# Optimization experiments

Hardware: AMD Instinct MI355X
Metric: run time of the kernel (lower is better)

The kernel has to match this reference:

```python
import jax, jax.numpy as jnp
import numpy as np

THRESHOLD = 0.3

def ternary_ste(w, threshold=THRESHOLD):
    # hard threshold to {-1, 0, +1}; straight-through in bwd via stop_gradient trick
    q = jnp.where(w > threshold, 1.0, jnp.where(w < -threshold, -1.0, 0.0)).astype(w.dtype)
    return w + jax.lax.stop_gradient(q - w)

def setup_inputs() -> dict:
    key = jax.random.key(0)
    k1, k2 = jax.random.split(key)
    x = jax.random.normal(k1, (16, 4096, 512), dtype=jnp.float32)
    weight = jax.random.normal(k2, (512, 512), dtype=jnp.float32) * 0.1  # nn.Parameter(randn*0.1)
    return {"x": x, "weight": weight}

def reference(x, weight):
    qw = ternary_ste(weight)  # [out_dim, in_dim]
    # F.linear(x, W) == x @ W.T
    return jnp.einsum('bsi,oi->bso', x, qw)
```

## Files before the change

kernel.cpp:

```cpp
#include <hip/hip_runtime.h>


#define TH    0.3f
#define NSLOT 16
#define ROWS  16
#define HALF  8
#define KDIM  512
#define NDIM  512

__global__ __launch_bounds__(64) void build_tbl(const float* __restrict__ w,
                                                int* __restrict__ counts,
                                                int* __restrict__ tbl) {
    const int o    = blockIdx.x;
    const int lane = threadIdx.x;
    __shared__ int c;
    __shared__ int se[KDIM];
    if (lane == 0) c = 0;
    __syncthreads();
    const float* row = w + (size_t)o * KDIM;
    for (int i = lane; i < KDIM; i += 64) {
        float v = row[i];
        if (v > TH || v < -TH) {
            int pos = atomicAdd(&c, 1);
            se[pos] = (i << 1) | (v < 0.0f ? 1 : 0);
        }
    }
    __syncthreads();
    const int cnt = c;
    if (lane == 0) counts[o] = cnt;
    for (int k = lane; k < NSLOT; k += 64)
        tbl[o * NSLOT + k] = (k < cnt) ? se[k] : 0;
}

__global__ __launch_bounds__(512) void sort_cols(const int* __restrict__ counts,
                                                 const int* __restrict__ tbl,
                                                 int* __restrict__ perm,
                                                 int* __restrict__ scnt,
                                                 int* __restrict__ stbl) {
    const int t = threadIdx.x;
    const int cnt = counts[t];
    const int key = cnt < (NSLOT + 1) ? cnt : (NSLOT + 1);
    __shared__ int base[NSLOT + 2];
    if (t < NSLOT + 2) base[t] = 0;
    __syncthreads();
    atomicAdd(&base[key], 1);
    __syncthreads();
    if (t == 0) {
        int run = 0;
        for (int c2 = NSLOT + 1; c2 >= 0; --c2) { int h = base[c2]; base[c2] = run; run += h; }
    }
    __syncthreads();
    const int pos = atomicAdd(&base[key], 1);
    perm[pos] = t;
    scnt[pos] = cnt;
#pragma unroll
    for (int k = 0; k < NSLOT; ++k) stbl[pos * NSLOT + k] = tbl[t * NSLOT + k];
}

__global__ __launch_bounds__(512, 8) void ternary_mm(
        const float* __restrict__ x, const float* __restrict__ w,
        const int* __restrict__ perm, const int* __restrict__ scnt,
        const int* __restrict__ stbl, float* __restrict__ out, int ntiles) {
    __shared__ float xs[ROWS * KDIM];

    const int t  = threadIdx.x;
    const int c  = perm[t];
    const int ct = scnt[t];
    int e[NSLOT];
#pragma unroll
    for (int k = 0; k < NSLOT; ++k) e[k] = stbl[t * NSLOT + k];

    const int fast = (ct <= NSLOT) ? ct : 0;
    int wm = fast;
#pragma unroll
    for (int off = 32; off; off >>= 1) { int o2 = __shfl_xor(wm, off); wm = wm > o2 ? wm : o2; }
    wm = __builtin_amdgcn_readfirstlane(wm);

    for (int tile = blockIdx.x; tile < ntiles; tile += gridDim.x) {
        const size_t base = (size_t)tile * (ROWS * KDIM);

        __syncthreads();
        {
            const float4* src = (const float4*)(x + base);
            float4 st0 = src[0 * 512 + t];
            float4 st1 = src[1 * 512 + t];
            float4 st2 = src[2 * 512 + t];
            float4 st3 = src[3 * 512 + t];
            float4* dst = (float4*)xs;
            dst[0 * 512 + t] = st0;
            dst[1 * 512 + t] = st1;
            dst[2 * 512 + t] = st2;
            dst[3 * 512 + t] = st3;
        }
        __syncthreads();

#pragma unroll
        for (int h = 0; h < 2; ++h) {
            float acc[HALF];
#pragma unroll
            for (int r = 0; r < HALF; ++r) acc[r] = 0.0f;

            if (ct <= NSLOT) {
#pragma unroll
                for (int k = 0; k < NSLOT; ++k) {
                    if (k >= wm) break;
                    if (k < fast) {
                        const int ent  = e[k];
                        const int idx  = ent >> 1;
                        const int smsk = (ent & 1) << 31;
#pragma unroll
                        for (int r = 0; r < HALF; ++r) {
                            float v = xs[(h * HALF + r) * KDIM + idx];
                            acc[r] += __int_as_float(__float_as_int(v) ^ smsk);
                        }
                    }
                }
            } else {
                const float* wrow = w + (size_t)c * KDIM;
                for (int i = 0; i < KDIM; ++i) {
                    float wv = wrow[i];
                    if (wv > TH || wv < -TH) {
                        const int smsk = (wv < 0.0f) ? (1 << 31) : 0;
#pragma unroll
                        for (int r = 0; r < HALF; ++r) {
                            float v = xs[(h * HALF + r) * KDIM + i];
                            acc[r] += __int_as_float(__float_as_int(v) ^ smsk);
                        }
                    }
                }
            }

            __syncthreads();
#pragma unroll
            for (int r = 0; r < HALF; ++r)
                xs[(h * HALF + r) * KDIM + c] = acc[r];
        }
        __syncthreads();

        {
            float4* dst = (float4*)(out + base);
            const float4* s4 = (const float4*)xs;
            dst[0 * 512 + t] = s4[0 * 512 + t];
            dst[1 * 512 + t] = s4[1 * 512 + t];
            dst[2 * 512 + t] = s4[2 * 512 + t];
            dst[3 * 512 + t] = s4[3 * 512 + t];
        }
    }
}

extern "C" void kernel_launch(void* const* d_in, const int* in_sizes, int n_in,
                              void* d_out, int out_size, void* d_ws, size_t ws_size,
                              hipStream_t stream) {
    const float* x = (const float*)d_in[0];
    const float* w = (const float*)d_in[1];
    float* out = (float*)d_out;

    int* counts = (int*)d_ws;
    int* tbl    = counts + NDIM;
    int* perm   = tbl + NDIM * NSLOT;
    int* scnt   = perm + NDIM;
    int* stbl   = scnt + NDIM;

    const int nrows  = in_sizes[0] / KDIM;
    const int ntiles = nrows / ROWS;

    build_tbl<<<NDIM, 64, 0, stream>>>(w, counts, tbl);
    sort_cols<<<1, 512, 0, stream>>>(counts, tbl, perm, scnt, stbl);
    ternary_mm<<<1024, 512, 0, stream>>>(x, w, perm, scnt, stbl, out, ntiles);
}
```

Baseline: 250.0 us.

## Fuse weight prep into one kernel and process full tiles per block

The two preprocessing kernels become one single-block kernel. It uses wave ballots and popcount to build the sparse ternary tables, then sorts the output columns by nonzero count. The main kernel no longer grid-strides: it launches one block per 16-row tile and accumulates all 16 rows in one pass instead of two halves, which removes extra barriers and raises per-thread ILP. Output is written with nontemporal stores. The trade-offs are higher register pressure from 16 accumulators and a serial single-block prep that could add latency.

```diff
diff --git a/kernel.cpp b/kernel.cpp
--- a/kernel.cpp
+++ b/kernel.cpp
@@ -4,63 +4,61 @@
 #define TH    0.3f
 #define NSLOT 16
 #define ROWS  16
-#define HALF  8
 #define KDIM  512
 #define NDIM  512
 
-__global__ __launch_bounds__(64) void build_tbl(const float* __restrict__ w,
-                                                int* __restrict__ counts,
-                                                int* __restrict__ tbl) {
-    const int o    = blockIdx.x;
-    const int lane = threadIdx.x;
-    __shared__ int c;
-    __shared__ int se[KDIM];
-    if (lane == 0) c = 0;
+typedef float floatx4 __attribute__((ext_vector_type(4)));
+
+__global__ __launch_bounds__(512) void prep(const float* __restrict__ w,
+                                            int* __restrict__ perm,
+                                            int* __restrict__ scnt,
+                                            int* __restrict__ stbl,
+                                            int* __restrict__ tbl) {
+    const int t    = threadIdx.x;
+    const int lane = t & 63;
+    const int wv   = t >> 6;
+    __shared__ int counts[NDIM];
+    __shared__ int hist[NSLOT + 2];
+
+    for (int r = wv * 64; r < wv * 64 + 64; ++r) {
+        const float* row = w + (size_t)r * KDIM;
+        int cnt = 0;
+        for (int it = 0; it < 8; ++it) {
+            const int i = it * 64 + lane;
+            const float v = row[i];
+            const bool m = (v > TH) || (v < -TH);
+            const unsigned long long mask = __ballot(m);
+            if (m) {
+                int pos = cnt + __popcll(mask & ((1ull << lane) - 1ull));
+                if (pos < NSLOT) tbl[r * NSLOT + pos] = (i << 1) | (v < 0.0f ? 1 : 0);
+            }
+            cnt += __popcll(mask);
+        }
+        if (lane == 0) counts[r] = cnt;
+        if (lane >= cnt && lane < NSLOT) tbl[r * NSLOT + lane] = 0;
+    }
+    if (t < NSLOT + 2) hist[t] = 0;
     __syncthreads();
-    const float* row = w + (size_t)o * KDIM;
-    for (int i = lane; i < KDIM; i += 64) {
-        float v = row[i];
-        if (v > TH || v < -TH) {
-            int pos = atomicAdd(&c, 1);
-            se[pos] = (i << 1) | (v < 0.0f ? 1 : 0);
-        }
-    }
-    __syncthreads();
-    const int cnt = c;
-    if (lane == 0) counts[o] = cnt;
-    for (int k = lane; k < NSLOT; k += 64)
-        tbl[o * NSLOT + k] = (k < cnt) ? se[k] : 0;
-}
 
-__global__ __launch_bounds__(512) void sort_cols(const int* __restrict__ counts,
-                                                 const int* __restrict__ tbl,
-                                                 int* __restrict__ perm,
-                                                 int* __restrict__ scnt,
-                                                 int* __restrict__ stbl) {
-    const int t = threadIdx.x;
     const int cnt = counts[t];
-    const int key = cnt < (NSLOT + 1) ? cnt : (NSLOT + 1);
-    __shared__ int base[NSLOT + 2];
-    if (t < NSLOT + 2) base[t] = 0;
-    __syncthreads();
-    atomicAdd(&base[key], 1);
+    const int key = cnt < NSLOT + 1 ? cnt : NSLOT + 1;
+    atomicAdd(&hist[key], 1);
     __syncthreads();
     if (t == 0) {
         int run = 0;
-        for (int c2 = NSLOT + 1; c2 >= 0; --c2) { int h = base[c2]; base[c2] = run; run += h; }
+        for (int k = NSLOT + 1; k >= 0; --k) { int h = hist[k]; hist[k] = run; run += h; }
     }
     __syncthreads();
-    const int pos = atomicAdd(&base[key], 1);
+    const int pos = atomicAdd(&hist[key], 1);
     perm[pos] = t;
     scnt[pos] = cnt;
-#pragma unroll
     for (int k = 0; k < NSLOT; ++k) stbl[pos * NSLOT + k] = tbl[t * NSLOT + k];
 }
 
 __global__ __launch_bounds__(512, 8) void ternary_mm(
         const float* __restrict__ x, const float* __restrict__ w,
         const int* __restrict__ perm, const int* __restrict__ scnt,
-        const int* __restrict__ stbl, float* __restrict__ out, int ntiles) {
+        const int* __restrict__ stbl, float* __restrict__ out) {
     __shared__ float xs[ROWS * KDIM];
 
     const int t  = threadIdx.x;
@@ -76,75 +74,64 @@
     for (int off = 32; off; off >>= 1) { int o2 = __shfl_xor(wm, off); wm = wm > o2 ? wm : o2; }
     wm = __builtin_amdgcn_readfirstlane(wm);
 
-    for (int tile = blockIdx.x; tile < ntiles; tile += gridDim.x) {
-        const size_t base = (size_t)tile * (ROWS * KDIM);
+    const size_t base = (size_t)blockIdx.x * (ROWS * KDIM);
 
-        __syncthreads();
-        {
-            const float4* src = (const float4*)(x + base);
-            float4 st0 = src[0 * 512 + t];
-            float4 st1 = src[1 * 512 + t];
-            float4 st2 = src[2 * 512 + t];
-            float4 st3 = src[3 * 512 + t];
-            float4* dst = (float4*)xs;
-            dst[0 * 512 + t] = st0;
-            dst[1 * 512 + t] = st1;
-            dst[2 * 512 + t] = st2;
-            dst[3 * 512 + t] = st3;
-        }
-        __syncthreads();
+    {
+        const floatx4* src = (const floatx4*)(x + base);
+        floatx4 a0 = src[0 * 512 + t], a1 = src[1 * 512 + t];
+        floatx4 a2 = src[2 * 512 + t], a3 = src[3 * 512 + t];
+        floatx4* dst = (floatx4*)xs;
+        dst[0 * 512 + t] = a0; dst[1 * 512 + t] = a1;
+        dst[2 * 512 + t] = a2; dst[3 * 512 + t] = a3;
+    }
+    __syncthreads();
 
+    float acc[ROWS];
 #pragma unroll
-        for (int h = 0; h < 2; ++h) {
-            float acc[HALF];
+    for (int r = 0; r < ROWS; ++r) acc[r] = 0.0f;
+
+    if (ct <= NSLOT) {
 #pragma unroll
-            for (int r = 0; r < HALF; ++r) acc[r] = 0.0f;
-
-            if (ct <= NSLOT) {
+        for (int k = 0; k < NSLOT; ++k) {
+            if (k >= wm) break;
+            if (k < fast) {
+                const int idx = e[k] >> 1;
+                const int sm  = (e[k] & 1) << 31;
 #pragma unroll
-                for (int k = 0; k < NSLOT; ++k) {
-                    if (k >= wm) break;
-                    if (k < fast) {
-                        const int ent  = e[k];
-                        const int idx  = ent >> 1;
-                        const int smsk = (ent & 1) << 31;
-#pragma unroll
-                        for (int r = 0; r < HALF; ++r) {
-                            float v = xs[(h * HALF + r) * KDIM + idx];
-                            acc[r] += __int_as_float(__float_as_int(v) ^ smsk);
-                        }
-                    }
-                }
-            } else {
-                const float* wrow = w + (size_t)c * KDIM;
-                for (int i = 0; i < KDIM; ++i) {
-                    float wv = wrow[i];
-                    if (wv > TH || wv < -TH) {
-                        const int smsk = (wv < 0.0f) ? (1 << 31) : 0;
-#pragma unroll
-                        for (int r = 0; r < HALF; ++r) {
-                            float v = xs[(h * HALF + r) * KDIM + i];
-                            acc[r] += __int_as_float(__float_as_int(v) ^ smsk);
-                        }
-                    }
+                for (int r = 0; r < ROWS; ++r) {
+                    float v = xs[r * KDIM + idx];
+                    acc[r] += __int_as_float(__float_as_int(v) ^ sm);
                 }
             }
+        }
+    } else {
+        const float* wrow = w + (size_t)c * KDIM;
+        for (int i = 0; i < KDIM; ++i) {
+            const float wv = wrow[i];
+            if (wv > TH || wv < -TH) {
+                const int sm = (wv < 0.0f) ? (1 << 31) : 0;
+#pragma unroll
+                for (int r = 0; r < ROWS; ++r) {
+                    float v = xs[r * KDIM + i];
+                    acc[r] += __int_as_float(__float_as_int(v) ^ sm);
+                }
+            }
+        }
+    }
 
-            __syncthreads();
+    __syncthreads();
 #pragma unroll
-            for (int r = 0; r < HALF; ++r)
-                xs[(h * HALF + r) * KDIM + c] = acc[r];
-        }
-        __syncthreads();
+    for (int r = 0; r < ROWS; ++r)
+        xs[r * KDIM + c] = acc[r];
+    __syncthreads();
 
-        {
-            float4* dst = (float4*)(out + base);
-            const float4* s4 = (const float4*)xs;
-            dst[0 * 512 + t] = s4[0 * 512 + t];
-            dst[1 * 512 + t] = s4[1 * 512 + t];
-            dst[2 * 512 + t] = s4[2 * 512 + t];
-            dst[3 * 512 + t] = s4[3 * 512 + t];
-        }
+    {
+        floatx4* dst = (floatx4*)(out + base);
+        const floatx4* s4 = (const floatx4*)xs;
+        __builtin_nontemporal_store(s4[0 * 512 + t], &dst[0 * 512 + t]);
+        __builtin_nontemporal_store(s4[1 * 512 + t], &dst[1 * 512 + t]);
+        __builtin_nontemporal_store(s4[2 * 512 + t], &dst[2 * 512 + t]);
+        __builtin_nontemporal_store(s4[3 * 512 + t], &dst[3 * 512 + t]);
     }
 }
 
@@ -155,16 +142,14 @@
     const float* w = (const float*)d_in[1];
     float* out = (float*)d_out;
 
-    int* counts = (int*)d_ws;
-    int* tbl    = counts + NDIM;
-    int* perm   = tbl + NDIM * NSLOT;
-    int* scnt   = perm + NDIM;
-    int* stbl   = scnt + NDIM;
+    int* perm = (int*)d_ws;
+    int* scnt = perm + NDIM;
+    int* stbl = scnt + NDIM;
+    int* tbl  = stbl + NDIM * NSLOT;
 
     const int nrows  = in_sizes[0] / KDIM;
     const int ntiles = nrows / ROWS;
 
-    build_tbl<<<NDIM, 64, 0, stream>>>(w, counts, tbl);
-    sort_cols<<<1, 512, 0, stream>>>(counts, tbl, perm, scnt, stbl);
-    ternary_mm<<<1024, 512, 0, stream>>>(x, w, perm, scnt, stbl, out, ntiles);
+    prep<<<1, 512, 0, stream>>>(w, perm, scnt, stbl, tbl);
+    ternary_mm<<<ntiles, 512, 0, stream>>>(x, w, perm, scnt, stbl, out);
 }
```

Measured after the change: 459.8 us. +83.9%, slower.
